# Kernel optimization log

Measured on AMD Instinct MI355X. Metric: run time of the kernel, lower is better.

The kernel has to match this reference:

```python
import jax, jax.numpy as jnp
import numpy as np

D = 256       # hp.encoder_dim
F = 256       # hp.duration_predictor_filter_size
K = 3         # hp.duration_predictor_kernel_size
ALPHA = 1.0
EPS = 1e-5


def _conv1d(x, w):
    # x: [N, L, Cin], w: [K, Cin, Cout], 'same' padding=1 for K=3
    return jax.lax.conv_general_dilated(
        x, w, window_strides=(1,), padding=((1, 1),),
        dimension_numbers=('NWC', 'WIO', 'NWC'))


def _layer_norm(h, g, b):
    mu = jnp.mean(h, axis=-1, keepdims=True)
    var = jnp.var(h, axis=-1, keepdims=True)
    return (h - mu) * jax.lax.rsqrt(var + EPS) * g + b


def setup_inputs() -> dict:
    key = jax.random.key(0)
    ks = jax.random.split(key, 12)
    N, L = 16, 512
    xavier_cw = float(np.sqrt(2.0 / (D * K + F * K)))  # xavier-ish for conv
    xavier_lw = float(np.sqrt(2.0 / (F + 1)))
    return {
        'x': jax.random.normal(ks[0], (N, L, D), dtype=jnp.float32),
        'conv1_w': jax.random.normal(ks[1], (K, D, F), dtype=jnp.float32) * xavier_cw,
        'conv1_b': jnp.zeros((F,), dtype=jnp.float32),
        'ln1_g': jnp.ones((F,), dtype=jnp.float32),
        'ln1_b': jnp.zeros((F,), dtype=jnp.float32),
        'conv2_w': jax.random.normal(ks[2], (K, F, F), dtype=jnp.float32) * xavier_cw,
        'conv2_b': jnp.zeros((F,), dtype=jnp.float32),
        'ln2_g': jnp.ones((F,), dtype=jnp.float32),
        'ln2_b': jnp.zeros((F,), dtype=jnp.float32),
        'lin_w': jax.random.normal(ks[3], (F, 1), dtype=jnp.float32) * xavier_lw,
        'lin_b': jnp.zeros((1,), dtype=jnp.float32),
        'WVF_max_length': 4096,
    }


def reference(x, conv1_w, conv1_b, ln1_g, ln1_b, conv2_w, conv2_b,
              ln2_g, ln2_b, lin_w, lin_b, WVF_max_length):
    # ---- DurationPredictor (eval mode: dropout = identity) ----
    h = _conv1d(x, conv1_w) + conv1_b            # [N, L, F]
    h = jax.nn.relu(_layer_norm(h, ln1_g, ln1_b))
    h = _conv1d(h, conv2_w) + conv2_b
    h = jax.nn.relu(_layer_norm(h, ln2_g, ln2_b))
    dpo = jax.nn.relu(h @ lin_w + lin_b)[..., 0]  # [N, L]

    # ---- LengthRegulator (no attn): int durations, alignment @ x ----
    dur = ((dpo + 0.5) * ALPHA).astype(jnp.int32)  # [N, L]
    ends = jnp.cumsum(dur, axis=-1)                # inclusive cumsum
    starts = ends - dur                            # exclusive cumsum
    t = jnp.arange(WVF_max_length)                 # static output length
    # alignment[n, t, l] = 1 iff starts[n,l] <= t < ends[n,l]
    align = ((t[None, :, None] >= starts[:, None, :]) &
             (t[None, :, None] < ends[:, None, :])).astype(x.dtype)  # [N, T, L]
    out = jnp.einsum('ntl,nld->ntd', align, x)     # [N, T, D]

    WVF_pos = jnp.arange(1, WVF_max_length + 1, dtype=jnp.int64
                         if jax.config.jax_enable_x64 else jnp.int32)[None, :]
    return out, WVF_pos
```

## Files before the change

kernel.cpp:

```cpp
#include <hip/hip_runtime.h>
#include <math.h>

#define N_   16
#define L_   512
#define C_   256
#define T_   4096
#define EPSL 1e-5f
#define BM   32

typedef short short8 __attribute__((ext_vector_type(8)));
typedef float f32x4  __attribute__((ext_vector_type(4)));

__device__ __forceinline__ ushort f2bf(float f) {
    union { float f; unsigned u; } v; v.f = f;
    return (ushort)((v.u + 0x7FFF + ((v.u >> 16) & 1)) >> 16);
}

__global__ __launch_bounds__(256) void pack_w_kernel(
    const float* __restrict__ w1, const float* __restrict__ w2,
    ushort* __restrict__ bpk1, ushort* __restrict__ bpk2)
{
    int gid = blockIdx.x * 256 + threadIdx.x;
    const float* w  = (gid < 24576) ? w1 : w2;
    ushort* bpk     = (gid < 24576) ? bpk1 : bpk2;
    int g2 = gid & 24575;
    int lane = g2 & 63;
    int s    = (g2 >> 6) & 7;
    int cg   = (g2 >> 9) & 15;
    int karm = g2 >> 13;
    int cin0 = s * 32 + (lane >> 4) * 8;
    int cout = cg * 16 + (lane & 15);
    const float* src = w + (size_t)(karm * 256 + cin0) * 256 + cout;
    short8 o;
    #pragma unroll
    for (int e = 0; e < 8; ++e) o[e] = (short)f2bf(src[(size_t)e * 256]);
    *reinterpret_cast<short8*>(bpk + (size_t)g2 * 8) = o;
}

__global__ __launch_bounds__(1024) void fused_conv_kernel(
    const float* __restrict__ x,
    const ushort* __restrict__ bpk1, const ushort* __restrict__ bpk2,
    const float* __restrict__ b1, const float* __restrict__ g1, const float* __restrict__ be1,
    const float* __restrict__ b2, const float* __restrict__ g2, const float* __restrict__ be2,
    const float* __restrict__ lw, const float* __restrict__ lb,
    int* __restrict__ dur)
{
    __shared__ __align__(16) char xt[50 * 512];
    __shared__ __align__(16) char h1t[34 * 512];
    __shared__ float redS[16][48], redQ[16][48], redP[16][32];

    const int tid  = threadIdx.x;
    const int wv   = tid >> 6;
    const int lane = tid & 63;
    const int lg   = lane >> 4;
    const int lr   = lane & 15;
    const int n    = blockIdx.x >> 4;
    const int l0   = (blockIdx.x & 15) << 5;
    const int col  = wv * 16 + lr;

    for (int idx = tid; idx < 36 * 32; idx += 1024) {
        int r = idx >> 5, slot = idx & 31;
        int l = l0 - 2 + r;
        short8 vb = {0,0,0,0,0,0,0,0};
        if (l >= 0 && l < L_) {
            const float* src = x + (((size_t)(n * L_ + l)) << 8) + (slot << 3);
            f32x4 f0 = *reinterpret_cast<const f32x4*>(src);
            f32x4 f1 = *reinterpret_cast<const f32x4*>(src + 4);
            vb[0]=(short)f2bf(f0[0]); vb[1]=(short)f2bf(f0[1]);
            vb[2]=(short)f2bf(f0[2]); vb[3]=(short)f2bf(f0[3]);
            vb[4]=(short)f2bf(f1[0]); vb[5]=(short)f2bf(f1[1]);
            vb[6]=(short)f2bf(f1[2]); vb[7]=(short)f2bf(f1[3]);
        }
        *reinterpret_cast<short8*>(xt + r * 512 + ((slot ^ (r & 15)) << 4)) = vb;
    }
    __syncthreads();

    f32x4 a1[3] = {};
    #pragma unroll
    for (int karm = 0; karm < 3; ++karm) {
        const ushort* bb = bpk1 + ((size_t)(karm * 16 + wv)) * 4096 + lane * 8;
        short8 bfr[8];
        #pragma unroll
        for (int s = 0; s < 8; ++s)
            bfr[s] = *reinterpret_cast<const short8*>(bb + s * 512);
        #pragma unroll
        for (int s = 0; s < 8; ++s) {
            #pragma unroll
            for (int t = 0; t < 3; ++t) {
                int rA = 16 * t + lr + karm;
                short8 a = *reinterpret_cast<const short8*>(
                    xt + rA * 512 + ((((s << 2) + lg) ^ (rA & 15)) << 4));
                a1[t] = __builtin_amdgcn_mfma_f32_16x16x32_bf16(a, bfr[s], a1[t], 0, 0, 0);
            }
        }
    }

    const float cb1 = b1[col], cg1 = g1[col], ce1 = be1[col];
    {
        float sv[12], qv[12];
        #pragma unroll
        for (int t = 0; t < 3; ++t)
            #pragma unroll
            for (int j = 0; j < 4; ++j) {
                float h = a1[t][j] + cb1;
                sv[t*4+j] = h; qv[t*4+j] = h * h;
            }
        #pragma unroll
        for (int m = 1; m < 16; m <<= 1)
            #pragma unroll
            for (int k = 0; k < 12; ++k) {
                sv[k] += __shfl_xor(sv[k], m, 64);
                qv[k] += __shfl_xor(qv[k], m, 64);
            }
        if (lr == 0) {
            #pragma unroll
            for (int t = 0; t < 3; ++t)
                #pragma unroll
                for (int j = 0; j < 4; ++j) {
                    redS[wv][16*t + lg*4 + j] = sv[t*4+j];
                    redQ[wv][16*t + lg*4 + j] = qv[t*4+j];
                }
        }
    }
    __syncthreads();
    if (tid < 48) {
        float ss = 0.f, qq = 0.f;
        #pragma unroll
        for (int u = 0; u < 16; ++u) { ss += redS[u][tid]; qq += redQ[u][tid]; }
        float m_  = ss * (1.f / 256.f);
        float var = fmaxf(qq * (1.f / 256.f) - m_ * m_, 0.f);
        redS[0][tid] = m_;
        redQ[0][tid] = 1.0f / sqrtf(var + EPSL);
    }
    __syncthreads();

    #pragma unroll
    for (int t = 0; t < 3; ++t)
        #pragma unroll
        for (int j = 0; j < 4; ++j) {
            int hr = 16*t + lg*4 + j;
            if (hr < 34) {
                int hl = l0 - 1 + hr;
                float r = 0.f;
                if (hl >= 0 && hl < L_)
                    r = fmaxf((a1[t][j] + cb1 - redS[0][hr]) * redQ[0][hr] * cg1 + ce1, 0.f);
                *(ushort*)(h1t + hr*512 + (((col >> 3) ^ (hr & 15)) << 4) + (col & 7) * 2) = f2bf(r);
            }
        }
    __syncthreads();

    f32x4 c2[2] = {};
    #pragma unroll
    for (int karm = 0; karm < 3; ++karm) {
        const ushort* bb = bpk2 + ((size_t)(karm * 16 + wv)) * 4096 + lane * 8;
        short8 bfr[8];
        #pragma unroll
        for (int s = 0; s < 8; ++s)
            bfr[s] = *reinterpret_cast<const short8*>(bb + s * 512);
        #pragma unroll
        for (int s = 0; s < 8; ++s) {
            #pragma unroll
            for (int tt = 0; tt < 2; ++tt) {
                int rA = 16 * tt + lr + karm;
                short8 a = *reinterpret_cast<const short8*>(
                    h1t + rA * 512 + ((((s << 2) + lg) ^ (rA & 15)) << 4));
                c2[tt] = __builtin_amdgcn_mfma_f32_16x16x32_bf16(a, bfr[s], c2[tt], 0, 0, 0);
            }
        }
    }

    const float cb2 = b2[col], cg2 = g2[col], ce2 = be2[col], clw = lw[col];
    {
        float sv[8], qv[8];
        #pragma unroll
        for (int tt = 0; tt < 2; ++tt)
            #pragma unroll
            for (int j = 0; j < 4; ++j) {
                float h = c2[tt][j] + cb2;
                sv[tt*4+j] = h; qv[tt*4+j] = h * h;
            }
        #pragma unroll
        for (int m = 1; m < 16; m <<= 1)
            #pragma unroll
            for (int k = 0; k < 8; ++k) {
                sv[k] += __shfl_xor(sv[k], m, 64);
                qv[k] += __shfl_xor(qv[k], m, 64);
            }
        if (lr == 0) {
            #pragma unroll
            for (int tt = 0; tt < 2; ++tt)
                #pragma unroll
                for (int j = 0; j < 4; ++j) {
                    redS[wv][16*tt + lg*4 + j] = sv[tt*4+j];
                    redQ[wv][16*tt + lg*4 + j] = qv[tt*4+j];
                }
        }
    }
    __syncthreads();
    if (tid < 32) {
        float ss = 0.f, qq = 0.f;
        #pragma unroll
        for (int u = 0; u < 16; ++u) { ss += redS[u][tid]; qq += redQ[u][tid]; }
        float m_  = ss * (1.f / 256.f);
        float var = fmaxf(qq * (1.f / 256.f) - m_ * m_, 0.f);
        redS[0][tid] = m_;
        redQ[0][tid] = 1.0f / sqrtf(var + EPSL);
    }
    __syncthreads();

    {
        float pv[8];
        #pragma unroll
        for (int tt = 0; tt < 2; ++tt)
            #pragma unroll
            for (int j = 0; j < 4; ++j) {
                int r = 16*tt + lg*4 + j;
                float rl = fmaxf((c2[tt][j] + cb2 - redS[0][r]) * redQ[0][r] * cg2 + ce2, 0.f);
                pv[tt*4+j] = rl * clw;
            }
        #pragma unroll
        for (int m = 1; m < 16; m <<= 1)
            #pragma unroll
            for (int k = 0; k < 8; ++k)
                pv[k] += __shfl_xor(pv[k], m, 64);
        if (lr == 0) {
            #pragma unroll
            for (int tt = 0; tt < 2; ++tt)
                #pragma unroll
                for (int j = 0; j < 4; ++j)
                    redP[wv][16*tt + lg*4 + j] = pv[tt*4+j];
        }
    }
    __syncthreads();
    if (tid < 32) {
        float dot = lb[0];
        #pragma unroll
        for (int u = 0; u < 16; ++u) dot += redP[u][tid];
        dur[n * L_ + l0 + tid] = (int)(fmaxf(dot, 0.f) + 0.5f);
    }
}

__global__ __launch_bounds__(64) void scan_pos_kernel(
    const int* __restrict__ dur, int* __restrict__ ends, float* __restrict__ wpos)
{
    const int n = blockIdx.x, lane = threadIdx.x;
    #pragma unroll
    for (int k = 0; k < 4; ++k) {
        int i = n * 256 + k * 64 + lane;
        wpos[i] = (float)(i + 1);
    }
    const int* dsrc = dur + n * L_;
    int4 va = reinterpret_cast<const int4*>(dsrc)[lane * 2];
    int4 vb = reinterpret_cast<const int4*>(dsrc)[lane * 2 + 1];
    int p0 = va.x,      p1 = p0 + va.y, p2 = p1 + va.z, p3 = p2 + va.w;
    int p4 = p3 + vb.x, p5 = p4 + vb.y, p6 = p5 + vb.z, p7 = p6 + vb.w;
    int tot = p7;
    #pragma unroll
    for (int m = 1; m < 64; m <<= 1) {
        int tu = __shfl_up(tot, m, 64);
        if (lane >= m) tot += tu;
    }
    int off = tot - p7;
    int* edst = ends + n * L_;
    int4 o1 = make_int4(p0 + off, p1 + off, p2 + off, p3 + off);
    int4 o2 = make_int4(p4 + off, p5 + off, p6 + off, p7 + off);
    reinterpret_cast<int4*>(edst)[lane * 2]     = o1;
    reinterpret_cast<int4*>(edst)[lane * 2 + 1] = o2;
}

__global__ __launch_bounds__(512) void gather_kernel(
    const float* __restrict__ x, const int* __restrict__ ends,
    float* __restrict__ out)
{
    const int wid = threadIdx.x >> 6, lane = threadIdx.x & 63;
    const int row = blockIdx.x * 8 + wid;
    const int n = row >> 12;
    const int t = row & (T_ - 1);
    const int* e = ends + n * L_;
    const int total = e[L_ - 1];

    f32x4 v = {0.f, 0.f, 0.f, 0.f};
    if (t < total) {
        int p = 0;
        #pragma unroll
        for (int step = 256; step > 0; step >>= 1)
            if (p + step <= L_ && e[p + step - 1] <= t) p += step;
        v = reinterpret_cast<const f32x4*>(x + (((size_t)(n * L_ + p)) << 8))[lane];
    }
    __builtin_nontemporal_store(v, reinterpret_cast<f32x4*>(out + ((size_t)row << 8)) + lane);
}

extern "C" void kernel_launch(void* const* d_in, const int* in_sizes, int n_in,
                              void* d_out, int out_size, void* d_ws, size_t ws_size,
                              hipStream_t stream)
{
    const float* x   = (const float*)d_in[0];
    const float* w1  = (const float*)d_in[1];
    const float* b1  = (const float*)d_in[2];
    const float* g1  = (const float*)d_in[3];
    const float* be1 = (const float*)d_in[4];
    const float* w2  = (const float*)d_in[5];
    const float* b2  = (const float*)d_in[6];
    const float* g2  = (const float*)d_in[7];
    const float* be2 = (const float*)d_in[8];
    const float* lw  = (const float*)d_in[9];
    const float* lb  = (const float*)d_in[10];

    float* out = (float*)d_out;
    ushort* bpk1 = (ushort*)d_out;
    ushort* bpk2 = bpk1 + 196608;
    int* dur     = (int*)d_ws;
    int* ends    = dur + N_ * L_;

    pack_w_kernel<<<192, 256, 0, stream>>>(w1, w2, bpk1, bpk2);

    fused_conv_kernel<<<N_ * (L_ / BM), 1024, 0, stream>>>(
        x, bpk1, bpk2, b1, g1, be1, b2, g2, be2, lw, lb, dur);

    scan_pos_kernel<<<N_, 64, 0, stream>>>(dur, ends, out + (size_t)N_ * T_ * C_);

    gather_kernel<<<N_ * T_ / 8, 512, 0, stream>>>(x, ends, out);
}
```

Measured before the change: 42.03 us.

## Halve conv block waves, fuse scan into gather, move pos fill to pack

The fused conv kernel now runs 512 threads per block, with each wave computing two 16-column output groups. This halves the cross-wave LayerNorm reductions and reuses each A-fragment LDS read across two MFMAs. The separate scan kernel is removed: every gather block recomputes the per-batch prefix sum of durations into shared memory, and the WVF_pos fill moves into the weight-pack kernel. This saves one kernel launch and the global round-trip for the ends array, at the cost of redundant scans in all 8192 gather blocks and higher register pressure in the conv kernel.

```diff
diff --git a/kernel.cpp b/kernel.cpp
--- a/kernel.cpp
+++ b/kernel.cpp
@@ -18,9 +18,11 @@
 
 __global__ __launch_bounds__(256) void pack_w_kernel(
     const float* __restrict__ w1, const float* __restrict__ w2,
-    ushort* __restrict__ bpk1, ushort* __restrict__ bpk2)
+    ushort* __restrict__ bpk1, ushort* __restrict__ bpk2,
+    float* __restrict__ wpos)
 {
     int gid = blockIdx.x * 256 + threadIdx.x;
+    if (gid < T_) wpos[gid] = (float)(gid + 1);
     const float* w  = (gid < 24576) ? w1 : w2;
     ushort* bpk     = (gid < 24576) ? bpk1 : bpk2;
     int g2 = gid & 24575;
@@ -37,7 +39,7 @@
     *reinterpret_cast<short8*>(bpk + (size_t)g2 * 8) = o;
 }
 
-__global__ __launch_bounds__(1024) void fused_conv_kernel(
+__global__ __launch_bounds__(512, 4) void fused_conv_kernel(
     const float* __restrict__ x,
     const ushort* __restrict__ bpk1, const ushort* __restrict__ bpk2,
     const float* __restrict__ b1, const float* __restrict__ g1, const float* __restrict__ be1,
@@ -47,7 +49,7 @@
 {
     __shared__ __align__(16) char xt[50 * 512];
     __shared__ __align__(16) char h1t[34 * 512];
-    __shared__ float redS[16][48], redQ[16][48], redP[16][32];
+    __shared__ float redS[8][48], redQ[8][48], redP[8][32];
 
     const int tid  = threadIdx.x;
     const int wv   = tid >> 6;
@@ -56,9 +58,10 @@
     const int lr   = lane & 15;
     const int n    = blockIdx.x >> 4;
     const int l0   = (blockIdx.x & 15) << 5;
-    const int col  = wv * 16 + lr;
-
-    for (int idx = tid; idx < 36 * 32; idx += 1024) {
+    const int cg0  = wv * 2;
+    const int col0 = wv * 32 + lr, col1 = col0 + 16;
+
+    for (int idx = tid; idx < 36 * 32; idx += 512) {
         int r = idx >> 5, slot = idx & 31;
         int l = l0 - 2 + r;
         short8 vb = {0,0,0,0,0,0,0,0};
@@ -75,35 +78,45 @@
     }
     __syncthreads();
 
-    f32x4 a1[3] = {};
+    f32x4 a1t[3][2] = {};
     #pragma unroll
     for (int karm = 0; karm < 3; ++karm) {
-        const ushort* bb = bpk1 + ((size_t)(karm * 16 + wv)) * 4096 + lane * 8;
-        short8 bfr[8];
-        #pragma unroll
-        for (int s = 0; s < 8; ++s)
-            bfr[s] = *reinterpret_cast<const short8*>(bb + s * 512);
-        #pragma unroll
-        for (int s = 0; s < 8; ++s) {
-            #pragma unroll
-            for (int t = 0; t < 3; ++t) {
-                int rA = 16 * t + lr + karm;
-                short8 a = *reinterpret_cast<const short8*>(
-                    xt + rA * 512 + ((((s << 2) + lg) ^ (rA & 15)) << 4));
-                a1[t] = __builtin_amdgcn_mfma_f32_16x16x32_bf16(a, bfr[s], a1[t], 0, 0, 0);
-            }
-        }
-    }
-
-    const float cb1 = b1[col], cg1 = g1[col], ce1 = be1[col];
+        const ushort* bb = bpk1 + ((size_t)(karm * 16 + cg0)) * 4096 + lane * 8;
+        #pragma unroll
+        for (int half = 0; half < 2; ++half) {
+            short8 bf0[4], bf1[4];
+            #pragma unroll
+            for (int s4 = 0; s4 < 4; ++s4) {
+                int s = half * 4 + s4;
+                bf0[s4] = *reinterpret_cast<const short8*>(bb + s * 512);
+                bf1[s4] = *reinterpret_cast<const short8*>(bb + 4096 + s * 512);
+            }
+            #pragma unroll
+            for (int s4 = 0; s4 < 4; ++s4) {
+                int s = half * 4 + s4;
+                #pragma unroll
+                for (int t = 0; t < 3; ++t) {
+                    int rA = 16 * t + lr + karm;
+                    short8 a = *reinterpret_cast<const short8*>(
+                        xt + rA * 512 + ((((s << 2) + lg) ^ (rA & 15)) << 4));
+                    a1t[t][0] = __builtin_amdgcn_mfma_f32_16x16x32_bf16(a, bf0[s4], a1t[t][0], 0, 0, 0);
+                    a1t[t][1] = __builtin_amdgcn_mfma_f32_16x16x32_bf16(a, bf1[s4], a1t[t][1], 0, 0, 0);
+                }
+            }
+        }
+    }
+
+    const float cb10 = b1[col0], cb11 = b1[col1];
+    const float cg10 = g1[col0], cg11 = g1[col1];
+    const float ce10 = be1[col0], ce11 = be1[col1];
     {
         float sv[12], qv[12];
         #pragma unroll
         for (int t = 0; t < 3; ++t)
             #pragma unroll
             for (int j = 0; j < 4; ++j) {
-                float h = a1[t][j] + cb1;
-                sv[t*4+j] = h; qv[t*4+j] = h * h;
+                float h0 = a1t[t][0][j] + cb10, h1 = a1t[t][1][j] + cb11;
+                sv[t*4+j] = h0 + h1; qv[t*4+j] = h0 * h0 + h1 * h1;
             }
         #pragma unroll
         for (int m = 1; m < 16; m <<= 1)
@@ -126,7 +139,7 @@
     if (tid < 48) {
         float ss = 0.f, qq = 0.f;
         #pragma unroll
-        for (int u = 0; u < 16; ++u) { ss += redS[u][tid]; qq += redQ[u][tid]; }
+        for (int u = 0; u < 8; ++u) { ss += redS[u][tid]; qq += redQ[u][tid]; }
         float m_  = ss * (1.f / 256.f);
         float var = fmaxf(qq * (1.f / 256.f) - m_ * m_, 0.f);
         redS[0][tid] = m_;
@@ -141,43 +154,57 @@
             int hr = 16*t + lg*4 + j;
             if (hr < 34) {
                 int hl = l0 - 1 + hr;
-                float r = 0.f;
-                if (hl >= 0 && hl < L_)
-                    r = fmaxf((a1[t][j] + cb1 - redS[0][hr]) * redQ[0][hr] * cg1 + ce1, 0.f);
-                *(ushort*)(h1t + hr*512 + (((col >> 3) ^ (hr & 15)) << 4) + (col & 7) * 2) = f2bf(r);
-            }
-        }
-    __syncthreads();
-
-    f32x4 c2[2] = {};
+                float r0 = 0.f, r1 = 0.f;
+                if (hl >= 0 && hl < L_) {
+                    r0 = fmaxf((a1t[t][0][j] + cb10 - redS[0][hr]) * redQ[0][hr] * cg10 + ce10, 0.f);
+                    r1 = fmaxf((a1t[t][1][j] + cb11 - redS[0][hr]) * redQ[0][hr] * cg11 + ce11, 0.f);
+                }
+                *(ushort*)(h1t + hr*512 + (((col0 >> 3) ^ (hr & 15)) << 4) + (col0 & 7) * 2) = f2bf(r0);
+                *(ushort*)(h1t + hr*512 + (((col1 >> 3) ^ (hr & 15)) << 4) + (col1 & 7) * 2) = f2bf(r1);
+            }
+        }
+    __syncthreads();
+
+    f32x4 c2[2][2] = {};
     #pragma unroll
     for (int karm = 0; karm < 3; ++karm) {
-        const ushort* bb = bpk2 + ((size_t)(karm * 16 + wv)) * 4096 + lane * 8;
-        short8 bfr[8];
-        #pragma unroll
-        for (int s = 0; s < 8; ++s)
-            bfr[s] = *reinterpret_cast<const short8*>(bb + s * 512);
-        #pragma unroll
-        for (int s = 0; s < 8; ++s) {
-            #pragma unroll
-            for (int tt = 0; tt < 2; ++tt) {
-                int rA = 16 * tt + lr + karm;
-                short8 a = *reinterpret_cast<const short8*>(
-                    h1t + rA * 512 + ((((s << 2) + lg) ^ (rA & 15)) << 4));
-                c2[tt] = __builtin_amdgcn_mfma_f32_16x16x32_bf16(a, bfr[s], c2[tt], 0, 0, 0);
-            }
-        }
-    }
-
-    const float cb2 = b2[col], cg2 = g2[col], ce2 = be2[col], clw = lw[col];
+        const ushort* bb = bpk2 + ((size_t)(karm * 16 + cg0)) * 4096 + lane * 8;
+        #pragma unroll
+        for (int half = 0; half < 2; ++half) {
+            short8 bf0[4], bf1[4];
+            #pragma unroll
+            for (int s4 = 0; s4 < 4; ++s4) {
+                int s = half * 4 + s4;
+                bf0[s4] = *reinterpret_cast<const short8*>(bb + s * 512);
+                bf1[s4] = *reinterpret_cast<const short8*>(bb + 4096 + s * 512);
+            }
+            #pragma unroll
+            for (int s4 = 0; s4 < 4; ++s4) {
+                int s = half * 4 + s4;
+                #pragma unroll
+                for (int tt = 0; tt < 2; ++tt) {
+                    int rA = 16 * tt + lr + karm;
+                    short8 a = *reinterpret_cast<const short8*>(
+                        h1t + rA * 512 + ((((s << 2) + lg) ^ (rA & 15)) << 4));
+                    c2[tt][0] = __builtin_amdgcn_mfma_f32_16x16x32_bf16(a, bf0[s4], c2[tt][0], 0, 0, 0);
+                    c2[tt][1] = __builtin_amdgcn_mfma_f32_16x16x32_bf16(a, bf1[s4], c2[tt][1], 0, 0, 0);
+                }
+            }
+        }
+    }
+
+    const float cb20 = b2[col0], cb21 = b2[col1];
+    const float cg20 = g2[col0], cg21 = g2[col1];
+    const float ce20 = be2[col0], ce21 = be2[col1];
+    const float lw0  = lw[col0],  lw1  = lw[col1];
     {
         float sv[8], qv[8];
         #pragma unroll
         for (int tt = 0; tt < 2; ++tt)
             #pragma unroll
             for (int j = 0; j < 4; ++j) {
-                float h = c2[tt][j] + cb2;
-                sv[tt*4+j] = h; qv[tt*4+j] = h * h;
+                float h0 = c2[tt][0][j] + cb20, h1 = c2[tt][1][j] + cb21;
+                sv[tt*4+j] = h0 + h1; qv[tt*4+j] = h0 * h0 + h1 * h1;
             }
         #pragma unroll
         for (int m = 1; m < 16; m <<= 1)
@@ -200,7 +227,7 @@
     if (tid < 32) {
         float ss = 0.f, qq = 0.f;
         #pragma unroll
-        for (int u = 0; u < 16; ++u) { ss += redS[u][tid]; qq += redQ[u][tid]; }
+        for (int u = 0; u < 8; ++u) { ss += redS[u][tid]; qq += redQ[u][tid]; }
         float m_  = ss * (1.f / 256.f);
         float var = fmaxf(qq * (1.f / 256.f) - m_ * m_, 0.f);
         redS[0][tid] = m_;
@@ -215,8 +242,9 @@
             #pragma unroll
             for (int j = 0; j < 4; ++j) {
                 int r = 16*tt + lg*4 + j;
-                float rl = fmaxf((c2[tt][j] + cb2 - redS[0][r]) * redQ[0][r] * cg2 + ce2, 0.f);
-                pv[tt*4+j] = rl * clw;
+                float r0 = fmaxf((c2[tt][0][j] + cb20 - redS[0][r]) * redQ[0][r] * cg20 + ce20, 0.f);
+                float r1 = fmaxf((c2[tt][1][j] + cb21 - redS[0][r]) * redQ[0][r] * cg21 + ce21, 0.f);
+                pv[tt*4+j] = r0 * lw0 + r1 * lw1;
             }
         #pragma unroll
         for (int m = 1; m < 16; m <<= 1)
@@ -235,59 +263,51 @@
     if (tid < 32) {
         float dot = lb[0];
         #pragma unroll
-        for (int u = 0; u < 16; ++u) dot += redP[u][tid];
+        for (int u = 0; u < 8; ++u) dot += redP[u][tid];
         dur[n * L_ + l0 + tid] = (int)(fmaxf(dot, 0.f) + 0.5f);
     }
 }
 
-__global__ __launch_bounds__(64) void scan_pos_kernel(
-    const int* __restrict__ dur, int* __restrict__ ends, float* __restrict__ wpos)
-{
-    const int n = blockIdx.x, lane = threadIdx.x;
-    #pragma unroll
-    for (int k = 0; k < 4; ++k) {
-        int i = n * 256 + k * 64 + lane;
-        wpos[i] = (float)(i + 1);
-    }
-    const int* dsrc = dur + n * L_;
-    int4 va = reinterpret_cast<const int4*>(dsrc)[lane * 2];
-    int4 vb = reinterpret_cast<const int4*>(dsrc)[lane * 2 + 1];
-    int p0 = va.x,      p1 = p0 + va.y, p2 = p1 + va.z, p3 = p2 + va.w;
-    int p4 = p3 + vb.x, p5 = p4 + vb.y, p6 = p5 + vb.z, p7 = p6 + vb.w;
-    int tot = p7;
-    #pragma unroll
-    for (int m = 1; m < 64; m <<= 1) {
-        int tu = __shfl_up(tot, m, 64);
-        if (lane >= m) tot += tu;
-    }
-    int off = tot - p7;
-    int* edst = ends + n * L_;
-    int4 o1 = make_int4(p0 + off, p1 + off, p2 + off, p3 + off);
-    int4 o2 = make_int4(p4 + off, p5 + off, p6 + off, p7 + off);
-    reinterpret_cast<int4*>(edst)[lane * 2]     = o1;
-    reinterpret_cast<int4*>(edst)[lane * 2 + 1] = o2;
-}
-
 __global__ __launch_bounds__(512) void gather_kernel(
-    const float* __restrict__ x, const int* __restrict__ ends,
+    const float* __restrict__ x, const int* __restrict__ dur,
     float* __restrict__ out)
 {
+    __shared__ __align__(16) int se[L_];
     const int wid = threadIdx.x >> 6, lane = threadIdx.x & 63;
-    const int row = blockIdx.x * 8 + wid;
-    const int n = row >> 12;
-    const int t = row & (T_ - 1);
-    const int* e = ends + n * L_;
-    const int total = e[L_ - 1];
+    const int blk = blockIdx.x;
+    const int n = blk >> 9;
+
+    if (wid == 0) {
+        const int* dsrc = dur + n * L_;
+        int4 va = reinterpret_cast<const int4*>(dsrc)[lane * 2];
+        int4 vb = reinterpret_cast<const int4*>(dsrc)[lane * 2 + 1];
+        int p0 = va.x,      p1 = p0 + va.y, p2 = p1 + va.z, p3 = p2 + va.w;
+        int p4 = p3 + vb.x, p5 = p4 + vb.y, p6 = p5 + vb.z, p7 = p6 + vb.w;
+        int tot = p7;
+        #pragma unroll
+        for (int m = 1; m < 64; m <<= 1) {
+            int tu = __shfl_up(tot, m, 64);
+            if (lane >= m) tot += tu;
+        }
+        int off = tot - p7;
+        reinterpret_cast<int4*>(se)[lane * 2]     = make_int4(p0+off, p1+off, p2+off, p3+off);
+        reinterpret_cast<int4*>(se)[lane * 2 + 1] = make_int4(p4+off, p5+off, p6+off, p7+off);
+    }
+    __syncthreads();
+
+    const int t = ((blk & 511) << 3) + wid;
+    const int total = se[L_ - 1];
 
     f32x4 v = {0.f, 0.f, 0.f, 0.f};
     if (t < total) {
         int p = 0;
         #pragma unroll
         for (int step = 256; step > 0; step >>= 1)
-            if (p + step <= L_ && e[p + step - 1] <= t) p += step;
+            if (p + step <= L_ && se[p + step - 1] <= t) p += step;
         v = reinterpret_cast<const f32x4*>(x + (((size_t)(n * L_ + p)) << 8))[lane];
     }
-    __builtin_nontemporal_store(v, reinterpret_cast<f32x4*>(out + ((size_t)row << 8)) + lane);
+    __builtin_nontemporal_store(
+        v, reinterpret_cast<f32x4*>(out + (((size_t)(n * T_ + t)) << 8)) + lane);
 }
 
 extern "C" void kernel_launch(void* const* d_in, const int* in_sizes, int n_in,
@@ -310,14 +330,12 @@
     ushort* bpk1 = (ushort*)d_out;
     ushort* bpk2 = bpk1 + 196608;
     int* dur     = (int*)d_ws;
-    int* ends    = dur + N_ * L_;
-
-    pack_w_kernel<<<192, 256, 0, stream>>>(w1, w2, bpk1, bpk2);
-
-    fused_conv_kernel<<<N_ * (L_ / BM), 1024, 0, stream>>>(
+
+    pack_w_kernel<<<192, 256, 0, stream>>>(w1, w2, bpk1, bpk2,
+                                           out + (size_t)N_ * T_ * C_);
+
+    fused_conv_kernel<<<N_ * (L_ / BM), 512, 0, stream>>>(
         x, bpk1, bpk2, b1, g1, be1, b2, g2, be2, lw, lb, dur);
 
-    scan_pos_kernel<<<N_, 64, 0, stream>>>(dur, ends, out + (size_t)N_ * T_ * C_);
-
-    gather_kernel<<<N_ * T_ / 8, 512, 0, stream>>>(x, ends, out);
-}
+    gather_kernel<<<N_ * T_ / 8, 512, 0, stream>>>(x, dur, out);
+}
```

Result: no change. 41.21 us (-1.9%).
